# Performance work log

Measured on AMD Instinct MI355X. Metric: run time of the kernel, lower is better.

Reference implementation:

```python
import jax, jax.numpy as jnp
import numpy as np

HEADS = 12
HEAD_DIM = 64          # dim_out // heads = 768 // 12
Q_STRIDE = 4
WINDOW_SIZE = 16       # post-pool tokens per window; pre-pool = Q_STRIDE*WINDOW_SIZE = 64
DIM = 768
DIM_OUT = 768


def setup_inputs() -> dict:
    key = jax.random.key(0)
    k1, k2, k3 = jax.random.split(key, 3)
    B, N = 32, 3136
    x = jax.random.normal(k1, (B, N, DIM), dtype=jnp.float32)
    Wqkv = jax.random.normal(k2, (DIM, 3 * DIM_OUT), dtype=jnp.float32) * 0.02
    bqkv = jnp.zeros((3 * DIM_OUT,), dtype=jnp.float32)
    Wproj = jax.random.normal(k3, (DIM_OUT, DIM_OUT), dtype=jnp.float32) * 0.02
    bproj = jnp.zeros((DIM_OUT,), dtype=jnp.float32)
    return {"x": x, "Wqkv": Wqkv, "bqkv": bqkv, "Wproj": Wproj, "bproj": bproj}


def reference(x, Wqkv, bqkv, Wproj, bproj):
    B, N, _ = x.shape
    num_windows = N // (Q_STRIDE * WINDOW_SIZE)  # 49
    scale = HEAD_DIM ** (-0.5)

    # QKV projection (torch Linear uses x @ W^T; here Wqkv is stored [dim, 3*dim_out])
    qkv = x @ Wqkv + bqkv                                  # [B, N, 3*dim_out]
    # Same reshape as torch: windows are the inner split of the token axis
    qkv = qkv.reshape(B, N // num_windows, num_windows, 3, HEADS, HEAD_DIM)
    qkv = jnp.transpose(qkv, (3, 0, 4, 2, 1, 5))           # [3, B, h, w, t, d]
    q, k, v = qkv[0], qkv[1], qkv[2]                       # t = Q_STRIDE*WINDOW_SIZE

    # Query max-pooling over stride groups
    q = q.reshape(B, HEADS, num_windows, Q_STRIDE, WINDOW_SIZE, HEAD_DIM).max(axis=3)
    # q: [B, h, w, WINDOW_SIZE, d]

    # Scaled dot-product attention within each window
    logits = jnp.einsum('bhwqd,bhwkd->bhwqk', q, k) * scale
    attn = jax.nn.softmax(logits, axis=-1)
    o = jnp.einsum('bhwqk,bhwkd->bhwqd', attn, v)          # [B, h, w, q, d]

    # transpose(1,3) then flatten tokens, channels = heads*head_dim
    o = jnp.transpose(o, (0, 3, 2, 1, 4)).reshape(B, -1, DIM_OUT)
    return o @ Wproj + bproj
```

## Files before the change

kernel.cpp:

```cpp
#include <hip/hip_runtime.h>
#include <hip/hip_bf16.h>


typedef __bf16 bf16x8 __attribute__((ext_vector_type(8)));
typedef float f32x4 __attribute__((ext_vector_type(4)));
typedef unsigned short u16x8 __attribute__((ext_vector_type(8)));

#define GLOBAL_AS __attribute__((address_space(1)))
#define LDS_AS __attribute__((address_space(3)))

__device__ __forceinline__ unsigned short f2bf(float f) {
    unsigned u = __builtin_bit_cast(unsigned, f);
    u += 0x7FFFu + ((u >> 16) & 1u);
    return (unsigned short)(u >> 16);
}
__device__ __forceinline__ float bf2f(unsigned short h) {
    return __builtin_bit_cast(float, (unsigned)h << 16);
}

__device__ __forceinline__ void load16_to_lds(const void* g, void* l) {
    __builtin_amdgcn_global_load_lds((const GLOBAL_AS unsigned int*)g,
                                     (LDS_AS unsigned int*)l, 16, 0, 0);
}

__global__ __launch_bounds__(256)
void cvt_permute(const float* __restrict__ in,
                 unsigned short* __restrict__ out, int nRows) {
    const int u = blockIdx.x * blockDim.x + threadIdx.x;
    if (u >= nRows * 96) return;
    const int g = u / 96;
    const int c = u - g * 96;
    const int b  = g / 3136;
    const int nn = g - b * 3136;
    const int t  = nn / 49;
    const int w  = nn - t * 49;
    float4 f0 = ((const float4*)in)[(long)g * 192 + c * 2];
    float4 f1 = ((const float4*)in)[(long)g * 192 + c * 2 + 1];
    uint4 o;
    o.x = (unsigned)f2bf(f0.x) | ((unsigned)f2bf(f0.y) << 16);
    o.y = (unsigned)f2bf(f0.z) | ((unsigned)f2bf(f0.w) << 16);
    o.z = (unsigned)f2bf(f1.x) | ((unsigned)f2bf(f1.y) << 16);
    o.w = (unsigned)f2bf(f1.z) | ((unsigned)f2bf(f1.w) << 16);
    ((uint4*)out)[(long)(b * 3136 + w * 64 + t) * 96 + c] = o;
}

__global__ void transpose_cvt2(const float* __restrict__ W0,
                               unsigned short* __restrict__ T0,
                               const float* __restrict__ W1,
                               unsigned short* __restrict__ T1) {
    __shared__ float tile[32][33];
    int bxi = blockIdx.x;
    const float* W; unsigned short* Wt; int N;
    if (bxi < 72) { W = W0; Wt = T0; N = 2304; }
    else          { W = W1; Wt = T1; N = 768; bxi -= 72; }
    const int K = 768;
    int bx = bxi * 32;
    int by = blockIdx.y * 32;
    int tx = threadIdx.x & 31, ty = threadIdx.x >> 5;
    #pragma unroll
    for (int i = 0; i < 32; i += 8)
        tile[ty + i][tx] = W[(size_t)(by + ty + i) * N + bx + tx];
    __syncthreads();
    #pragma unroll
    for (int i = 0; i < 32; i += 8)
        Wt[(size_t)(bx + ty + i) * K + by + tx] = f2bf(tile[tx][ty + i]);
}

#define VM_WAIT2 asm volatile("s_waitcnt vmcnt(2)" ::: "memory")
#define VM_WAIT0 asm volatile("s_waitcnt vmcnt(0)" ::: "memory")

#define GPHASE(BUF, CSW, IH, LOADBG, STG, WAITS) do {                        \
    if (LOADBG) {                                                            \
        const unsigned short* bb = &ls[(BUF) * 32768 + 16384 + (CSW)];       \
        bg[0] = *(const bf16x8*)&bb[(wn +  0 + lane15) * 64];                \
        bg[1] = *(const bf16x8*)&bb[(wn + 16 + lane15) * 64];                \
        bg[2] = *(const bf16x8*)&bb[(wn + 32 + lane15) * 64];                \
        bg[3] = *(const bf16x8*)&bb[(wn + 48 + lane15) * 64];                \
    }                                                                        \
    {                                                                        \
        const unsigned short* ab = &ls[(BUF) * 32768 + (CSW)];               \
        af[0] = *(const bf16x8*)&ab[(wm + (IH)*64 +  0 + lane15) * 64];      \
        af[1] = *(const bf16x8*)&ab[(wm + (IH)*64 + 16 + lane15) * 64];      \
        af[2] = *(const bf16x8*)&ab[(wm + (IH)*64 + 32 + lane15) * 64];      \
        af[3] = *(const bf16x8*)&ab[(wm + (IH)*64 + 48 + lane15) * 64];      \
    }                                                                        \
    STG;                                                                     \
    WAITS;                                                                   \
    __builtin_amdgcn_s_barrier();                                            \
    asm volatile("s_waitcnt lgkmcnt(0)" ::: "memory");                       \
    __builtin_amdgcn_sched_barrier(0);                                       \
    __builtin_amdgcn_s_setprio(1);                                           \
    _Pragma("unroll")                                                        \
    for (int ii = 0; ii < 4; ++ii)                                           \
        _Pragma("unroll")                                                    \
        for (int j = 0; j < 4; ++j)                                          \
            acc[(IH)*4 + ii][j] = __builtin_amdgcn_mfma_f32_16x16x32_bf16(   \
                bg[j], af[ii], acc[(IH)*4 + ii][j], 0, 0, 0);                \
    __builtin_amdgcn_s_setprio(0);                                           \
    __builtin_amdgcn_s_barrier();                                            \
} while (0)

template <bool OUT_BF16>
__global__ __launch_bounds__(512, 2)
void gemm_bt256(const unsigned short* __restrict__ A,
                const unsigned short* __restrict__ Bt,
                const float* __restrict__ bias,
                void* __restrict__ Cv, int mBase, int N, int K) {
    __shared__ alignas(16) unsigned short ls[65536];

    const int tid  = threadIdx.x;
    const int lane = tid & 63;
    const int wave = tid >> 6;
    const int wm = (wave >> 2) * 128;
    const int wn = (wave & 3) * 64;
    const int lane15 = lane & 15;
    const int quad   = lane >> 4;
    const int csw0 = ((quad    ) ^ (lane & 7)) * 8;
    const int csw1 = ((quad + 4) ^ (lane & 7)) * 8;

    const int nwg = (int)(gridDim.x * gridDim.y);
    const int hid = (int)(blockIdx.y * gridDim.x + blockIdx.x);
    const int q8  = nwg >> 3, r8 = nwg & 7;
    const int xcd = hid & 7;
    const int lid = (xcd < r8 ? xcd * (q8 + 1) : r8 * (q8 + 1) + (xcd - r8) * q8)
                    + (hid >> 3);
    const int tileX = lid % (int)gridDim.x;
    const int tileY = lid / (int)gridDim.x;
    const long bm = (long)tileY * 256;
    const long bn = (long)tileX * 256;

    const int r0 = tid >> 3;
    const int lc = (tid & 7) ^ (r0 & 7);
    const unsigned short* gA = A  + (bm + r0) * (long)K + lc * 8;
    const unsigned short* gB = Bt + (bn + r0) * (long)K + lc * 8;
    const int ldsWaveBase = wave * 512;

    auto STAGE_A = [&](int buf, int q, int kt) {
        load16_to_lds(gA + (long)q * 64 * K + kt * 64,
                      &ls[buf * 32768 + q * 4096 + ldsWaveBase]);
    };
    auto STAGE_B = [&](int buf, int q, int kt) {
        load16_to_lds(gB + (long)q * 64 * K + kt * 64,
                      &ls[buf * 32768 + 16384 + q * 4096 + ldsWaveBase]);
    };

    f32x4 acc[8][4] = {};
    bf16x8 af[4], bg[4];

    const int NT = K >> 6;
    const int NI = NT >> 1;

    STAGE_A(0, 0, 0); STAGE_A(0, 1, 0); STAGE_A(0, 2, 0); STAGE_A(0, 3, 0);
    STAGE_B(0, 0, 0); STAGE_B(0, 1, 0); STAGE_B(0, 2, 0); STAGE_B(0, 3, 0);
    STAGE_A(1, 0, 1); STAGE_A(1, 2, 1);
    VM_WAIT2;
    __builtin_amdgcn_s_barrier();

    for (int i = 0; i < NI; ++i) {
        const int t2 = 2 * i;
        const bool last = (i == NI - 1);
        GPHASE(0, csw0, 0, 1,
               { STAGE_A(1, 1, t2 + 1); STAGE_A(1, 3, t2 + 1); STAGE_B(1, 0, t2 + 1); },
               { (void)0; });
        GPHASE(0, csw0, 1, 0,
               { STAGE_B(1, 1, t2 + 1); STAGE_B(1, 2, t2 + 1); STAGE_B(1, 3, t2 + 1); },
               { (void)0; });
        GPHASE(0, csw1, 0, 1, { (void)0; }, { (void)0; });
        GPHASE(0, csw1, 1, 0,
               { if (!last) { STAGE_A(0, 0, t2 + 2); STAGE_A(0, 2, t2 + 2); } },
               { if (last) { VM_WAIT0; } else { VM_WAIT2; } });
        GPHASE(1, csw0, 0, 1,
               { if (!last) { STAGE_A(0, 1, t2 + 2); STAGE_A(0, 3, t2 + 2); } },
               { (void)0; });
        GPHASE(1, csw0, 1, 0,
               { if (!last) { STAGE_B(0, 0, t2 + 2); STAGE_B(0, 1, t2 + 2); } },
               { (void)0; });
        GPHASE(1, csw1, 0, 1,
               { if (!last) { STAGE_B(0, 2, t2 + 2); STAGE_B(0, 3, t2 + 2); } },
               { (void)0; });
        GPHASE(1, csw1, 1, 0,
               { if (!last) { STAGE_A(1, 0, t2 + 3); STAGE_A(1, 2, t2 + 3); VM_WAIT2; } },
               { (void)0; });
    }

    const int rbase = (int)(bm) + wm + lane15;
    if constexpr (OUT_BF16) {
        const int colBase = (int)bn + wn;
        const int sec = colBase / 768;
        const int hh  = (colBase - sec * 768) >> 6;
        const long shOff = (long)sec * 49152 + hh * 4096 + quad * 4;
        unsigned short* qout = (unsigned short*)Cv;
        float4 bv[4];
        #pragma unroll
        for (int j = 0; j < 4; ++j)
            bv[j] = *(const float4*)&bias[colBase + quad * 4 + j * 16];
        #pragma unroll
        for (int i = 0; i < 8; ++i) {
            const int m  = mBase + rbase + i * 16;
            const int b  = m / 3136;
            const int r3 = m - b * 3136;
            unsigned short* rp = qout + (long)(b * 49 + (r3 >> 6)) * 147456
                                      + shOff + (long)(r3 & 63) * 64;
            #pragma unroll
            for (int j = 0; j < 4; ++j) {
                ushort4 s;
                s.x = f2bf(acc[i][j][0] + bv[j].x);
                s.y = f2bf(acc[i][j][1] + bv[j].y);
                s.z = f2bf(acc[i][j][2] + bv[j].z);
                s.w = f2bf(acc[i][j][3] + bv[j].w);
                *(ushort4*)(rp + j * 16) = s;
            }
        }
    } else {
        const int cbase = (int)bn + wn + quad * 4;
        #pragma unroll
        for (int j = 0; j < 4; ++j) {
            const int col = cbase + j * 16;
            const float4 bv = *(const float4*)&bias[col];
            #pragma unroll
            for (int i = 0; i < 8; ++i) {
                const long row = (long)mBase + rbase + i * 16;
                const size_t idx = (size_t)row * N + col;
                float4 s;
                s.x = acc[i][j][0] + bv.x;
                s.y = acc[i][j][1] + bv.y;
                s.z = acc[i][j][2] + bv.z;
                s.w = acc[i][j][3] + bv.w;
                *(float4*)((float*)Cv + idx) = s;
            }
        }
    }
}

__global__ __launch_bounds__(256, 4)
void attn_win_mfma(const unsigned short* __restrict__ qkv,
                   unsigned short* __restrict__ o) {
    const int hg = blockIdx.x;
    const int w  = blockIdx.y;
    const int b  = blockIdx.z;
    const int wave = threadIdx.x >> 6;
    const int lane = threadIdx.x & 63;
    const int h = hg * 4 + wave;
    const int l = lane & 15;
    const int quad = lane >> 4;

    __shared__ alignas(16) unsigned short vT[4][64 * 64];
    __shared__ alignas(16) unsigned short ps[4][16 * 64];

    const long slab = (long)(b * 49 + w) * 147456;
    const long hOff = (long)h * 4096;

    bf16x8 af[2];
    {
        const unsigned short* qr = qkv + slab + hOff + (long)l * 64 + quad * 8;
        float m0[8], m1[8];
        #pragma unroll
        for (int sg = 0; sg < 4; ++sg) {
            uint4 u0 = *(const uint4*)(qr + sg * 1024);
            uint4 u1 = *(const uint4*)(qr + sg * 1024 + 32);
            const unsigned short* p0 = (const unsigned short*)&u0;
            const unsigned short* p1 = (const unsigned short*)&u1;
            #pragma unroll
            for (int e = 0; e < 8; ++e) {
                float f0 = bf2f(p0[e]), f1 = bf2f(p1[e]);
                if (sg == 0) { m0[e] = f0; m1[e] = f1; }
                else { m0[e] = fmaxf(m0[e], f0); m1[e] = fmaxf(m1[e], f1); }
            }
        }
        u16x8 a0, a1;
        #pragma unroll
        for (int e = 0; e < 8; ++e) {
            a0[e] = f2bf(m0[e] * 0.125f);
            a1[e] = f2bf(m1[e] * 0.125f);
        }
        af[0] = __builtin_bit_cast(bf16x8, a0);
        af[1] = __builtin_bit_cast(bf16x8, a1);
    }

    {
        const unsigned short* vr = qkv + slab + 98304 + hOff + (long)lane * 64;
        unsigned short* vw = &vT[wave][0];
        const int ch = lane >> 3, le = lane & 7;
        #pragma unroll
        for (int i = 0; i < 8; ++i) {
            uint4 u = *(const uint4*)(vr + i * 8);
            const unsigned short* pe = (const unsigned short*)&u;
            #pragma unroll
            for (int e = 0; e < 8; ++e) {
                const int d = i * 8 + e;
                vw[d * 64 + ((ch ^ (d & 7)) << 3) + le] = pe[e];
            }
        }
    }

    f32x4 Sc[4] = {};
    {
        bf16x8 bk0, bk1;
        __builtin_amdgcn_s_setprio(1);
        #pragma unroll
        for (int tt = 0; tt < 4; ++tt) {
            const unsigned short* kr =
                qkv + slab + 49152 + hOff + (long)(tt * 16 + l) * 64 + quad * 8;
            bk0 = __builtin_bit_cast(bf16x8, *(const uint4*)kr);
            bk1 = __builtin_bit_cast(bf16x8, *(const uint4*)(kr + 32));
            Sc[tt] = __builtin_amdgcn_mfma_f32_16x16x32_bf16(af[0], bk0, Sc[tt], 0, 0, 0);
            Sc[tt] = __builtin_amdgcn_mfma_f32_16x16x32_bf16(af[1], bk1, Sc[tt], 0, 0, 0);
        }
        __builtin_amdgcn_s_setprio(0);
    }

    float pr[4][4];
    {
        #pragma unroll
        for (int r = 0; r < 4; ++r) {
            float mx = fmaxf(fmaxf(Sc[0][r], Sc[1][r]), fmaxf(Sc[2][r], Sc[3][r]));
            #pragma unroll
            for (int off = 1; off < 16; off <<= 1)
                mx = fmaxf(mx, __shfl_xor(mx, off));
            float sum = 0.f;
            #pragma unroll
            for (int tt = 0; tt < 4; ++tt) {
                pr[tt][r] = __expf(Sc[tt][r] - mx);
                sum += pr[tt][r];
            }
            #pragma unroll
            for (int off = 1; off < 16; off <<= 1)
                sum += __shfl_xor(sum, off);
            const float inv = 1.0f / sum;
            #pragma unroll
            for (int tt = 0; tt < 4; ++tt) pr[tt][r] *= inv;
        }
    }

    {
        unsigned short* pw = &ps[wave][0];
        #pragma unroll
        for (int r = 0; r < 4; ++r) {
            const int row = quad * 4 + r;
            #pragma unroll
            for (int tt = 0; tt < 4; ++tt) {
                const int c = (tt << 1) + (l >> 3);
                pw[row * 64 + ((c ^ (row & 7)) << 3) + (l & 7)] = f2bf(pr[tt][r]);
            }
        }
    }

    f32x4 Oc[4] = {};
    {
        __builtin_amdgcn_s_setprio(1);
        #pragma unroll
        for (int s = 0; s < 2; ++s) {
            const int csw = (((s << 2) + quad) ^ (l & 7)) << 3;
            bf16x8 ap = *(const bf16x8*)&ps[wave][l * 64 + csw];
            #pragma unroll
            for (int tt = 0; tt < 4; ++tt) {
                bf16x8 bv = *(const bf16x8*)&vT[wave][(tt * 16 + l) * 64 + csw];
                Oc[tt] = __builtin_amdgcn_mfma_f32_16x16x32_bf16(ap, bv, Oc[tt], 0, 0, 0);
            }
        }
        __builtin_amdgcn_s_setprio(0);
    }

    {
        const long obase = ((long)b * 784 + (long)(quad * 4) * 49 + w) * 768 + h * 64 + l;
        #pragma unroll
        for (int tt = 0; tt < 4; ++tt)
            #pragma unroll
            for (int r = 0; r < 4; ++r)
                o[obase + (long)r * 49 * 768 + tt * 16] = f2bf(Oc[tt][r]);
    }
}

extern "C" void kernel_launch(void* const* d_in, const int* in_sizes, int n_in,
                              void* d_out, int out_size, void* d_ws, size_t ws_size,
                              hipStream_t stream) {
    const float* x     = (const float*)d_in[0];
    const float* Wqkv  = (const float*)d_in[1];
    const float* bqkv  = (const float*)d_in[2];
    const float* Wproj = (const float*)d_in[3];
    const float* bproj = (const float*)d_in[4];
    float* out = (float*)d_out;

    const long needed1 = (32L * 3136 * 768 + 32L * 3136 * 2304 +
                          25088L * 768 + 2304L * 768 + 768L * 768) * 2;
    const int C  = (ws_size >= (size_t)needed1) ? 1 : 4;
    const int CB = 32 / C;
    const long XC = (long)CB * 3136 * 768;
    const long QC = (long)CB * 3136 * 2304;

    char* p = (char*)d_ws;
    unsigned short* xb    = (unsigned short*)p; p += XC * 2;
    unsigned short* qkvb  = (unsigned short*)p; p += QC * 2;
    unsigned short* ob    = (unsigned short*)p; p += 25088L * 768 * 2;
    unsigned short* WqkvT = (unsigned short*)p; p += 2304L * 768 * 2;
    unsigned short* WprojT= (unsigned short*)p; p += 768L * 768 * 2;

    transpose_cvt2<<<dim3(96, 24), 256, 0, stream>>>(Wqkv, WqkvT, Wproj, WprojT);

    const int M = CB * 3136;
    const int tiles = M / 256;
    const int tc0 = (tiles + 2) / 3;
    const int tc1 = (tiles - tc0 + 1) / 2;
    const int tc2 = tiles - tc0 - tc1;
    for (int c = 0; c < C; ++c) {
        cvt_permute<<<(M * 96 + 255) / 256, 256, 0, stream>>>(
            x + (size_t)c * XC, xb, M);
        int mb = 0;
        const int tcs[3] = {tc0, tc1, tc2};
        for (int s = 0; s < 3; ++s) {
            if (tcs[s] > 0)
                gemm_bt256<true><<<dim3(9, tcs[s]), 512, 0, stream>>>(
                    xb + (long)mb * 768, WqkvT, bqkv, qkvb, mb, 2304, 768);
            mb += tcs[s] * 256;
        }
        attn_win_mfma<<<dim3(3, 49, CB), 256, 0, stream>>>(
            qkvb, ob + (size_t)c * CB * 784 * 768);
    }
    gemm_bt256<false><<<dim3(3, 98), 512, 0, stream>>>(
        ob, WprojT, bproj, out, 0, 768, 768);
}
```

Before: 1.105 ms.

## Fold token permutation into QKV GEMM A-loads and merge GEMM launches

```diff
diff --git a/kernel.cpp b/kernel.cpp
--- a/kernel.cpp
+++ b/kernel.cpp
@@ -24,24 +24,18 @@
 }
 
 __global__ __launch_bounds__(256)
-void cvt_permute(const float* __restrict__ in,
-                 unsigned short* __restrict__ out, int nRows) {
-    const int u = blockIdx.x * blockDim.x + threadIdx.x;
-    if (u >= nRows * 96) return;
-    const int g = u / 96;
-    const int c = u - g * 96;
-    const int b  = g / 3136;
-    const int nn = g - b * 3136;
-    const int t  = nn / 49;
-    const int w  = nn - t * 49;
-    float4 f0 = ((const float4*)in)[(long)g * 192 + c * 2];
-    float4 f1 = ((const float4*)in)[(long)g * 192 + c * 2 + 1];
+void cvt_f32_bf16(const float* __restrict__ in,
+                  unsigned short* __restrict__ out, long n8) {
+    const long i = (long)blockIdx.x * blockDim.x + threadIdx.x;
+    if (i >= n8) return;
+    float4 f0 = ((const float4*)in)[i * 2];
+    float4 f1 = ((const float4*)in)[i * 2 + 1];
     uint4 o;
     o.x = (unsigned)f2bf(f0.x) | ((unsigned)f2bf(f0.y) << 16);
     o.y = (unsigned)f2bf(f0.z) | ((unsigned)f2bf(f0.w) << 16);
     o.z = (unsigned)f2bf(f1.x) | ((unsigned)f2bf(f1.y) << 16);
     o.w = (unsigned)f2bf(f1.z) | ((unsigned)f2bf(f1.w) << 16);
-    ((uint4*)out)[(long)(b * 3136 + w * 64 + t) * 96 + c] = o;
+    ((uint4*)out)[i] = o;
 }
 
 __global__ void transpose_cvt2(const float* __restrict__ W0,
@@ -66,6 +60,7 @@
         Wt[(size_t)(bx + ty + i) * K + by + tx] = f2bf(tile[tx][ty + i]);
 }
 
+#define VM_WAIT3 asm volatile("s_waitcnt vmcnt(3)" ::: "memory")
 #define VM_WAIT2 asm volatile("s_waitcnt vmcnt(2)" ::: "memory")
 #define VM_WAIT0 asm volatile("s_waitcnt vmcnt(0)" ::: "memory")
 
@@ -100,12 +95,12 @@
     __builtin_amdgcn_s_barrier();                                            \
 } while (0)
 
-template <bool OUT_BF16>
+template <bool QKV>
 __global__ __launch_bounds__(512, 2)
 void gemm_bt256(const unsigned short* __restrict__ A,
                 const unsigned short* __restrict__ Bt,
                 const float* __restrict__ bias,
-                void* __restrict__ Cv, int mBase, int N, int K) {
+                void* __restrict__ Cv, int N, int K) {
     __shared__ alignas(16) unsigned short ls[65536];
 
     const int tid  = threadIdx.x;
@@ -131,12 +126,25 @@
 
     const int r0 = tid >> 3;
     const int lc = (tid & 7) ^ (r0 & 7);
-    const unsigned short* gA = A  + (bm + r0) * (long)K + lc * 8;
+    const unsigned short* gAq[4];
+    #pragma unroll
+    for (int q = 0; q < 4; ++q) {
+        const int mq = (int)bm + q * 64 + r0;
+        long srow;
+        if constexpr (QKV) {
+            const int b  = mq / 3136;
+            const int r3 = mq - b * 3136;
+            srow = (long)b * 3136 + (long)(r3 & 63) * 49 + (r3 >> 6);
+        } else {
+            srow = mq;
+        }
+        gAq[q] = A + srow * (long)K + lc * 8;
+    }
     const unsigned short* gB = Bt + (bn + r0) * (long)K + lc * 8;
     const int ldsWaveBase = wave * 512;
 
     auto STAGE_A = [&](int buf, int q, int kt) {
-        load16_to_lds(gA + (long)q * 64 * K + kt * 64,
+        load16_to_lds(gAq[q] + kt * 64,
                       &ls[buf * 32768 + q * 4096 + ldsWaveBase]);
     };
     auto STAGE_B = [&](int buf, int q, int kt) {
@@ -167,24 +175,24 @@
                { (void)0; });
         GPHASE(0, csw1, 0, 1, { (void)0; }, { (void)0; });
         GPHASE(0, csw1, 1, 0,
-               { if (!last) { STAGE_A(0, 0, t2 + 2); STAGE_A(0, 2, t2 + 2); } },
-               { if (last) { VM_WAIT0; } else { VM_WAIT2; } });
+               { if (!last) { STAGE_B(0, 0, t2 + 2); STAGE_B(0, 1, t2 + 2);
+                              STAGE_B(0, 2, t2 + 2); } },
+               { if (last) { VM_WAIT0; } else { VM_WAIT3; } });
         GPHASE(1, csw0, 0, 1,
+               { if (!last) { STAGE_B(0, 3, t2 + 2); STAGE_A(0, 0, t2 + 2);
+                              STAGE_A(0, 2, t2 + 2); } },
+               { (void)0; });
+        GPHASE(1, csw0, 1, 0,
                { if (!last) { STAGE_A(0, 1, t2 + 2); STAGE_A(0, 3, t2 + 2); } },
                { (void)0; });
-        GPHASE(1, csw0, 1, 0,
-               { if (!last) { STAGE_B(0, 0, t2 + 2); STAGE_B(0, 1, t2 + 2); } },
-               { (void)0; });
-        GPHASE(1, csw1, 0, 1,
-               { if (!last) { STAGE_B(0, 2, t2 + 2); STAGE_B(0, 3, t2 + 2); } },
-               { (void)0; });
+        GPHASE(1, csw1, 0, 1, { (void)0; }, { (void)0; });
         GPHASE(1, csw1, 1, 0,
                { if (!last) { STAGE_A(1, 0, t2 + 3); STAGE_A(1, 2, t2 + 3); VM_WAIT2; } },
                { (void)0; });
     }
 
     const int rbase = (int)(bm) + wm + lane15;
-    if constexpr (OUT_BF16) {
+    if constexpr (QKV) {
         const int colBase = (int)bn + wn;
         const int sec = colBase / 768;
         const int hh  = (colBase - sec * 768) >> 6;
@@ -196,7 +204,7 @@
             bv[j] = *(const float4*)&bias[colBase + quad * 4 + j * 16];
         #pragma unroll
         for (int i = 0; i < 8; ++i) {
-            const int m  = mBase + rbase + i * 16;
+            const int m  = rbase + i * 16;
             const int b  = m / 3136;
             const int r3 = m - b * 3136;
             unsigned short* rp = qout + (long)(b * 49 + (r3 >> 6)) * 147456
@@ -219,7 +227,7 @@
             const float4 bv = *(const float4*)&bias[col];
             #pragma unroll
             for (int i = 0; i < 8; ++i) {
-                const long row = (long)mBase + rbase + i * 16;
+                const long row = (long)rbase + i * 16;
                 const size_t idx = (size_t)row * N + col;
                 float4 s;
                 s.x = acc[i][j][0] + bv.x;
@@ -398,24 +406,14 @@
     transpose_cvt2<<<dim3(96, 24), 256, 0, stream>>>(Wqkv, WqkvT, Wproj, WprojT);
 
     const int M = CB * 3136;
-    const int tiles = M / 256;
-    const int tc0 = (tiles + 2) / 3;
-    const int tc1 = (tiles - tc0 + 1) / 2;
-    const int tc2 = tiles - tc0 - tc1;
     for (int c = 0; c < C; ++c) {
-        cvt_permute<<<(M * 96 + 255) / 256, 256, 0, stream>>>(
-            x + (size_t)c * XC, xb, M);
-        int mb = 0;
-        const int tcs[3] = {tc0, tc1, tc2};
-        for (int s = 0; s < 3; ++s) {
-            if (tcs[s] > 0)
-                gemm_bt256<true><<<dim3(9, tcs[s]), 512, 0, stream>>>(
-                    xb + (long)mb * 768, WqkvT, bqkv, qkvb, mb, 2304, 768);
-            mb += tcs[s] * 256;
-        }
+        cvt_f32_bf16<<<(int)((M * 96L + 255) / 256), 256, 0, stream>>>(
+            x + (size_t)c * XC, xb, M * 96L);
+        gemm_bt256<true><<<dim3(9, M / 256), 512, 0, stream>>>(
+            xb, WqkvT, bqkv, qkvb, 2304, 768);
         attn_win_mfma<<<dim3(3, 49, CB), 256, 0, stream>>>(
             qkvb, ob + (size_t)c * CB * 784 * 768);
     }
     gemm_bt256<false><<<dim3(3, 98), 512, 0, stream>>>(
-        ob, WprojT, bproj, out, 0, 768, 768);
-}
+        ob, WprojT, bproj, out, 768, 768);
+}
```

Measured after the change: 1.059 ms. -4.2%, faster.
